# Optimization experiments

Measured on AMD Instinct MI355X. Metric: run time of the kernel, lower is better.

The kernel has to match this reference:

```python
import jax, jax.numpy as jnp
import numpy as np

N = 6144
D = 128
TAU = 0.1
ADJ_P = 0.005  # edge density


def _l2_normalize(x, eps=1e-12):
    # matches torch F.normalize: x / max(||x||, eps)
    n = jnp.sqrt(jnp.sum(x * x, axis=-1, keepdims=True))
    return x / jnp.maximum(n, eps)


def setup_inputs() -> dict:
    key = jax.random.key(0)
    ks = jax.random.split(key, 8)
    embF = jax.random.normal(ks[0], (N, D), jnp.float32)
    embM = jax.random.normal(ks[1], (N, D), jnp.float32)
    embP = jax.random.normal(ks[2], (N, D), jnp.float32)
    FM_adj = (jax.random.uniform(ks[3], (N, N)) < ADJ_P).astype(jnp.float32)
    FP_adj = (jax.random.uniform(ks[4], (N, N)) < ADJ_P).astype(jnp.float32)
    W1 = jax.random.normal(ks[5], (2 * D, D), jnp.float32) * (1.0 / np.sqrt(2 * D))
    b1 = jnp.zeros((D,), jnp.float32)
    W2 = jax.random.normal(ks[6], (D, 2), jnp.float32) * (1.0 / np.sqrt(D))
    b2 = jnp.zeros((2,), jnp.float32)
    return {"embF": embF, "embM": embM, "embP": embP,
            "FM_adj": FM_adj, "FP_adj": FP_adj,
            "W1": W1, "b1": b1, "W2": W2, "b2": b2}


def reference(embF, embM, embP, FM_adj, FP_adj, W1, b1, W2, b2):
    # attention-weighted neighbor aggregation
    FM_repr = (FM_adj @ embM) / jnp.maximum(FM_adj.sum(1, keepdims=True), 1.0)
    FP_repr = (FP_adj @ embP) / jnp.maximum(FP_adj.sum(1, keepdims=True), 1.0)
    # stack(dim=1).view(N,-1) == concat along feature dim
    feat = jnp.concatenate([FM_repr, FP_repr], axis=1)            # [N, 2D]
    h = jnp.maximum(feat @ W1 + b1, 0.0)                           # ReLU (dropout inactive in eval)
    weights = jax.nn.softmax(h @ W2 + b2, axis=-1)                 # [N, 2]

    Fn = _l2_normalize(embF)
    Mn = _l2_normalize(embM)
    Pn = _l2_normalize(embP)

    FM_sim = jnp.exp((Fn @ Mn.T) / TAU)                            # [N, Nm]
    FP_sim = jnp.exp((Fn @ Pn.T) / TAU)                            # [N, Np]

    FM_pos = jnp.sum(FM_sim * FM_adj, axis=1)
    FP_pos = jnp.sum(FP_sim * FP_adj, axis=1)
    FM_neg = jnp.sum(FM_sim, axis=1) - FM_pos
    FP_neg = jnp.sum(FP_sim, axis=1) - FP_pos

    w0, w1w = weights[:, 0], weights[:, 1]
    wp = w0 * FM_pos + w1w * FP_pos
    wn = w0 * FM_neg + w1w * FP_neg

    nei_count = jnp.maximum(FM_adj.sum(1) + FP_adj.sum(1), 1.0)
    ratio = wp / (wp + wn) / nei_count
    ratio = jnp.maximum(ratio, 1e-10)
    loss = jnp.mean(-jnp.log(ratio))
    return loss, weights
```

## Files before the change

### kernel.cpp

```cpp
#include <hip/hip_runtime.h>
#include <hip/hip_bf16.h>

#define NN 6144
#define DD 128
#define PBL 136
#define INV_TAU 10.0f

typedef __attribute__((ext_vector_type(4))) float f32x4;
typedef __attribute__((ext_vector_type(8))) short s16x8;

__device__ __forceinline__ void ld4_async(const float4* p, float4& d) {
    asm volatile("global_load_dwordx4 %0, %1, off" : "=v"(d) : "v"(p));
}
__device__ __forceinline__ void vm_wait0() {
    asm volatile("s_waitcnt vmcnt(0)" ::: "memory");
}

__global__ void k_normalize(const float* __restrict__ embF,
                            const float* __restrict__ embM,
                            const float* __restrict__ embP,
                            const float* __restrict__ W1,
                            float* __restrict__ Fn,
                            float* __restrict__ rnM, float* __restrict__ rnP,
                            __hip_bfloat16* __restrict__ Fnb,
                            __hip_bfloat16* __restrict__ Mnb,
                            __hip_bfloat16* __restrict__ Pnb,
                            __hip_bfloat16* __restrict__ W1tb,
                            float* __restrict__ FMtot,
                            float* __restrict__ out) {
    int which = blockIdx.y;
    if (which == 3) {
        if (blockIdx.x < 128) {
            int n = blockIdx.x, c = threadIdx.x;
            W1tb[n * 256 + c] = __float2bfloat16(W1[c * DD + n]);
        } else if (blockIdx.x < 176) {
            int i = (blockIdx.x - 128) * 256 + threadIdx.x;
            FMtot[i] = 0.f;
        } else if (blockIdx.x == 176 && threadIdx.x == 0) {
            out[0] = 0.f;
        }
        return;
    }
    const float* src = which == 0 ? embF : (which == 1 ? embM : embP);
    __hip_bfloat16* dstb = which == 0 ? Fnb : (which == 1 ? Mnb : Pnb);
    int wave = threadIdx.x >> 6, lane = threadIdx.x & 63;
    int row = blockIdx.x * 4 + wave;
    float2 v = reinterpret_cast<const float2*>(src + (size_t)row * DD)[lane];
    float s = v.x * v.x + v.y * v.y;
#pragma unroll
    for (int m = 1; m <= 32; m <<= 1) s += __shfl_xor(s, m);
    float inv = 1.0f / fmaxf(sqrtf(s), 1e-12f);
    float2 o; o.x = v.x * inv; o.y = v.y * inv;
    if (which == 0)
        reinterpret_cast<float2*>(Fn + (size_t)row * DD)[lane] = o;
    if (lane == 0) {
        if (which == 1) rnM[row] = inv;
        if (which == 2) rnP[row] = inv;
    }
    __hip_bfloat162 ob;
    ob.x = __float2bfloat16(o.x);
    ob.y = __float2bfloat16(o.y);
    reinterpret_cast<__hip_bfloat162*>(dstb + (size_t)row * DD)[lane] = ob;
}

__device__ __forceinline__ void sparse_body(
        int unit, char* smem,
        const float* __restrict__ FM_adj, const float* __restrict__ FP_adj,
        const float* __restrict__ embM, const float* __restrict__ embP,
        const float* __restrict__ Fn,
        const float* __restrict__ rnM, const float* __restrict__ rnP,
        __hip_bfloat16* __restrict__ featb,
        float* __restrict__ FMpos, float* __restrict__ FPpos,
        float* __restrict__ cntF, float* __restrict__ cntP) {
    float* FnS = (float*)smem;
    int (*lbufT)[5] = (int(*)[5])(smem + 512);
    int* listS = (int*)(smem + 512 + 5120);
    float (*reprS)[DD] = (float(*)[DD])(smem + 512 + 5120 + 512);
    float* posS = (float*)(smem + 512 + 5120 + 512 + 4096);
    int* wvS = (int*)(smem + 512 + 5120 + 512 + 4096 + 32);
    int* Ktot = (int*)(smem + 512 + 5120 + 512 + 4096 + 32 + 16);

    const int row = unit >> 1, h = unit & 1;
    const float* adj  = h ? FP_adj : FM_adj;
    const float* embX = h ? embP : embM;
    const float* RN   = h ? rnP : rnM;
    const int tid = threadIdx.x, wv = tid >> 6, lane = tid & 63;

    if (tid < 32)
        reinterpret_cast<float4*>(FnS)[tid] =
            reinterpret_cast<const float4*>(Fn + (size_t)row * DD)[tid];

    const float4* rp = reinterpret_cast<const float4*>(adj + (size_t)row * NN);
    float4 v0, v1, v2, v3, v4, v5;
    ld4_async(rp + tid,        v0);
    ld4_async(rp + 256 + tid,  v1);
    ld4_async(rp + 512 + tid,  v2);
    ld4_async(rp + 768 + tid,  v3);
    ld4_async(rp + 1024 + tid, v4);
    ld4_async(rp + 1280 + tid, v5);
    vm_wait0();
    float4 vv[6] = {v0, v1, v2, v3, v4, v5};
    int mycnt = 0;
#pragma unroll
    for (int u = 0; u < 6; ++u) {
        int cb = (u * 256 + tid) * 4;
        if (vv[u].x != 0.f) { if (mycnt < 4) lbufT[tid][mycnt] = cb;     mycnt++; }
        if (vv[u].y != 0.f) { if (mycnt < 4) lbufT[tid][mycnt] = cb + 1; mycnt++; }
        if (vv[u].z != 0.f) { if (mycnt < 4) lbufT[tid][mycnt] = cb + 2; mycnt++; }
        if (vv[u].w != 0.f) { if (mycnt < 4) lbufT[tid][mycnt] = cb + 3; mycnt++; }
    }
    int cnt = mycnt < 4 ? mycnt : 4;
    int x = cnt;
#pragma unroll
    for (int d = 1; d < 64; d <<= 1) {
        int y = __shfl_up(x, d);
        if (lane >= d) x += y;
    }
    int t = mycnt;
#pragma unroll
    for (int msk = 1; msk <= 32; msk <<= 1) t += __shfl_xor(t, msk);
    if (tid == 0) Ktot[1] = 0;
    if (lane == 63) wvS[wv] = x;
    __syncthreads();
    if (lane == 0) atomicAdd(&Ktot[1], t);
    if (tid == 0) {
        int s = 0;
#pragma unroll
        for (int i = 0; i < 4; ++i) { int v = wvS[i]; wvS[i] = s; s += v; }
        Ktot[0] = s < 128 ? s : 128;
    }
    __syncthreads();
    int off = wvS[wv] + (x - cnt);
    for (int i = 0; i < cnt; ++i) {
        int s = off + i;
        if (s < 128) listS[s] = lbufT[tid][i];
    }
    __syncthreads();
    const int K = Ktot[0];
    const float trueK = (float)Ktot[1];

    const int hw = tid >> 5, sl = tid & 31;
    float4 f4 = reinterpret_cast<const float4*>(FnS)[sl];
    float4 racc = {0.f, 0.f, 0.f, 0.f};
    float wsum = 0.f;
    for (int k = hw; k < K; k += 8) {
        int j = listS[k];
        float rn = RN[j];
        float4 e = reinterpret_cast<const float4*>(embX + (size_t)j * DD)[sl];
        racc.x += e.x; racc.y += e.y; racc.z += e.z; racc.w += e.w;
        float d = f4.x * e.x + f4.y * e.y + f4.z * e.z + f4.w * e.w;
#pragma unroll
        for (int msk = 1; msk <= 16; msk <<= 1) d += __shfl_xor(d, msk);
        wsum += __expf(d * rn * INV_TAU);
    }
    reinterpret_cast<float4*>(&reprS[hw][0])[sl] = racc;
    if (sl == 0) posS[hw] = wsum;
    __syncthreads();
    if (tid < DD) {
        float s = 0.f;
#pragma unroll
        for (int i = 0; i < 8; ++i) s += reprS[i][tid];
        featb[(size_t)row * (2 * DD) + h * DD + tid] =
            __float2bfloat16(s / fmaxf(trueK, 1.0f));
    }
    if (tid == 0) {
        float p = 0.f;
#pragma unroll
        for (int i = 0; i < 8; ++i) p += posS[i];
        (h ? FPpos : FMpos)[row] = p;
        (h ? cntP : cntF)[row] = trueK;
    }
}

__device__ __forceinline__ void dense_body(
        int unit, char* smem,
        const __hip_bfloat16* __restrict__ Fnb,
        const __hip_bfloat16* __restrict__ Mnb,
        const __hip_bfloat16* __restrict__ Pnb,
        float* __restrict__ FMtot, float* __restrict__ FPtot) {
    __hip_bfloat16 (*Bs)[PBL] = (__hip_bfloat16(*)[PBL])smem;
    const int bx = unit % 48, by = (unit / 48) % 16, half = unit / 768;
    const __hip_bfloat16* Bnb = half ? Pnb : Mnb;
    float* TOT = half ? FPtot : FMtot;
    const int tid = threadIdx.x;
    const int w = tid >> 6, lane = tid & 63;
    const int m = lane & 15, q = lane >> 4;
    const int rb = bx * 128 + w * 32;
    const int j0 = by * (NN / 16);

    s16x8 a[2][4];
#pragma unroll
    for (int g = 0; g < 2; ++g)
#pragma unroll
        for (int ks = 0; ks < 4; ++ks)
            a[g][ks] = *reinterpret_cast<const s16x8*>(
                Fnb + (size_t)(rb + g * 16 + m) * DD + ks * 32 + q * 8);

    float4 s0, s1, s2, s3;
    auto issue = [&](int jc) {
        const float4* gp = reinterpret_cast<const float4*>(Bnb + (size_t)jc * DD);
        ld4_async(gp + tid,       s0);
        ld4_async(gp + 256 + tid, s1);
        ld4_async(gp + 512 + tid, s2);
        ld4_async(gp + 768 + tid, s3);
    };
    auto stash = [&](int idx, const float4& v) {
        *reinterpret_cast<float4*>(&Bs[idx >> 4][(idx & 15) * 8]) = v;
    };

    issue(j0);
    float tot[2][4] = {{0.f, 0.f, 0.f, 0.f}, {0.f, 0.f, 0.f, 0.f}};
    for (int it = 0; it < 6; ++it) {
        vm_wait0();
        __syncthreads();
        stash(tid, s0);
        stash(256 + tid, s1);
        stash(512 + tid, s2);
        stash(768 + tid, s3);
        __syncthreads();
        if (it + 1 < 6) issue(j0 + (it + 1) * 64);
#pragma unroll
        for (int t = 0; t < 4; ++t) {
            s16x8 b[4];
#pragma unroll
            for (int ks = 0; ks < 4; ++ks)
                b[ks] = *reinterpret_cast<const s16x8*>(
                    &Bs[t * 16 + m][ks * 32 + q * 8]);
#pragma unroll
            for (int g = 0; g < 2; ++g) {
                f32x4 acc = {0.f, 0.f, 0.f, 0.f};
#pragma unroll
                for (int ks = 0; ks < 4; ++ks)
                    acc = __builtin_amdgcn_mfma_f32_16x16x32_bf16(
                        a[g][ks], b[ks], acc, 0, 0, 0);
#pragma unroll
                for (int r = 0; r < 4; ++r)
                    tot[g][r] += __expf(acc[r] * INV_TAU);
            }
        }
    }
#pragma unroll
    for (int msk = 1; msk <= 8; msk <<= 1)
#pragma unroll
        for (int g = 0; g < 2; ++g)
#pragma unroll
            for (int r = 0; r < 4; ++r)
                tot[g][r] += __shfl_xor(tot[g][r], msk);
    if (m == 0)
#pragma unroll
        for (int g = 0; g < 2; ++g)
#pragma unroll
            for (int r = 0; r < 4; ++r)
                atomicAdd(&TOT[rb + g * 16 + q * 4 + r], tot[g][r]);
}

__global__ __launch_bounds__(256) void k_main(
        const float* __restrict__ FM_adj, const float* __restrict__ FP_adj,
        const float* __restrict__ embM, const float* __restrict__ embP,
        const float* __restrict__ Fn,
        const float* __restrict__ rnM, const float* __restrict__ rnP,
        const __hip_bfloat16* __restrict__ Fnb,
        const __hip_bfloat16* __restrict__ Mnb,
        const __hip_bfloat16* __restrict__ Pnb,
        __hip_bfloat16* __restrict__ featb,
        float* __restrict__ FMpos, float* __restrict__ FPpos,
        float* __restrict__ FMtot, float* __restrict__ FPtot,
        float* __restrict__ cntF, float* __restrict__ cntP) {
    __shared__ char smem[64 * PBL * 2];
    const int b = blockIdx.x;
    const int u = b / 9, r = b - u * 9;
    if (r == 8)
        dense_body(u, smem, Fnb, Mnb, Pnb, FMtot, FPtot);
    else
        sparse_body(u * 8 + r, smem, FM_adj, FP_adj, embM, embP,
                    Fn, rnM, rnP, featb, FMpos, FPpos, cntF, cntP);
}

__global__ __launch_bounds__(256) void k_post(
        const __hip_bfloat16* __restrict__ featb,
        const __hip_bfloat16* __restrict__ W1tb,
        const float* __restrict__ b1, const float* __restrict__ W2,
        const float* __restrict__ b2,
        const float* __restrict__ FMpos, const float* __restrict__ FPpos,
        const float* __restrict__ FMtot, const float* __restrict__ FPtot,
        const float* __restrict__ cntF, const float* __restrict__ cntP,
        float* __restrict__ out) {
    __shared__ float zred[4][16][2];
    const int tid = threadIdx.x, w = tid >> 6, lane = tid & 63;
    const int m = lane & 15, q = lane >> 4;
    const int rb = blockIdx.x * 16;
    const int n0a = w * 32, n0b = w * 32 + 16;
    f32x4 accA = {0.f, 0.f, 0.f, 0.f}, accB = {0.f, 0.f, 0.f, 0.f};
#pragma unroll
    for (int ks = 0; ks < 8; ++ks) {
        s16x8 a = *reinterpret_cast<const s16x8*>(
            featb + (size_t)(rb + m) * 256 + ks * 32 + q * 8);
        s16x8 bA = *reinterpret_cast<const s16x8*>(
            W1tb + (size_t)(n0a + m) * 256 + ks * 32 + q * 8);
        s16x8 bB = *reinterpret_cast<const s16x8*>(
            W1tb + (size_t)(n0b + m) * 256 + ks * 32 + q * 8);
        accA = __builtin_amdgcn_mfma_f32_16x16x32_bf16(a, bA, accA, 0, 0, 0);
        accB = __builtin_amdgcn_mfma_f32_16x16x32_bf16(a, bB, accB, 0, 0, 0);
    }
    const float biasA = b1[n0a + m], biasB = b1[n0b + m];
    const float wA0 = W2[2 * (n0a + m)], wA1 = W2[2 * (n0a + m) + 1];
    const float wB0 = W2[2 * (n0b + m)], wB1 = W2[2 * (n0b + m) + 1];
#pragma unroll
    for (int r = 0; r < 4; ++r) {
        float hA = fmaxf(accA[r] + biasA, 0.f);
        float hB = fmaxf(accB[r] + biasB, 0.f);
        float p0 = hA * wA0 + hB * wB0;
        float p1 = hA * wA1 + hB * wB1;
#pragma unroll
        for (int msk = 1; msk <= 8; msk <<= 1) {
            p0 += __shfl_xor(p0, msk);
            p1 += __shfl_xor(p1, msk);
        }
        if (m == 0) {
            zred[w][q * 4 + r][0] = p0;
            zred[w][q * 4 + r][1] = p1;
        }
    }
    __syncthreads();
    if (tid < 16) {
        const int row = rb + tid;
        float z0 = zred[0][tid][0] + zred[1][tid][0]
                 + zred[2][tid][0] + zred[3][tid][0] + b2[0];
        float z1 = zred[0][tid][1] + zred[1][tid][1]
                 + zred[2][tid][1] + zred[3][tid][1] + b2[1];
        float mx = fmaxf(z0, z1);
        float e0 = expf(z0 - mx), e1 = expf(z1 - mx);
        float inv = 1.0f / (e0 + e1);
        float w0 = e0 * inv, w1 = e1 * inv;
        out[1 + row * 2 + 0] = w0;
        out[1 + row * 2 + 1] = w1;
        float wp = w0 * FMpos[row] + w1 * FPpos[row];
        float wn = w0 * (FMtot[row] - FMpos[row]) + w1 * (FPtot[row] - FPpos[row]);
        float nei = fmaxf(cntF[row] + cntP[row], 1.0f);
        float ratio = fmaxf(wp / (wp + wn) / nei, 1e-10f);
        float term = -logf(ratio);
#pragma unroll
        for (int msk = 1; msk <= 8; msk <<= 1) term += __shfl_xor(term, msk);
        if (tid == 0) atomicAdd(out, term * (1.0f / NN));
    }
}

extern "C" void kernel_launch(void* const* d_in, const int* in_sizes, int n_in,
                              void* d_out, int out_size, void* d_ws, size_t ws_size,
                              hipStream_t stream) {
    const float* embF   = (const float*)d_in[0];
    const float* embM   = (const float*)d_in[1];
    const float* embP   = (const float*)d_in[2];
    const float* FM_adj = (const float*)d_in[3];
    const float* FP_adj = (const float*)d_in[4];
    const float* W1     = (const float*)d_in[5];
    const float* b1     = (const float*)d_in[6];
    const float* W2     = (const float*)d_in[7];
    const float* b2     = (const float*)d_in[8];
    float* out = (float*)d_out;

    float* ws = (float*)d_ws;
    float* FMtot = ws;
    float* FPtot = FMtot + NN;
    float* zbuf  = FPtot + NN;
    float* FMpos = zbuf + 2 * NN;
    float* FPpos = FMpos + NN;
    float* cntF  = FPpos + NN;
    float* cntP  = cntF + NN;
    float* rnM   = cntP + NN;
    float* rnP   = rnM + NN;
    float* Fn    = rnP + NN;
    __hip_bfloat16* Fnb = (__hip_bfloat16*)(Fn + (size_t)NN * DD);
    __hip_bfloat16* Mnb = Fnb + (size_t)NN * DD;
    __hip_bfloat16* Pnb = Mnb + (size_t)NN * DD;
    __hip_bfloat16* featb = Pnb + (size_t)NN * DD;
    __hip_bfloat16* W1tb  = featb + (size_t)NN * 256;

    k_normalize<<<dim3(NN / 4, 4), 256, 0, stream>>>(embF, embM, embP, W1,
                                                     Fn, rnM, rnP,
                                                     Fnb, Mnb, Pnb, W1tb,
                                                     FMtot, out);
    k_main<<<dim3(13824), 256, 0, stream>>>(FM_adj, FP_adj, embM, embP,
                                            Fn, rnM, rnP, Fnb, Mnb, Pnb,
                                            featb, FMpos, FPpos, FMtot, FPtot,
                                            cntF, cntP);
    k_post<<<dim3(NN / 16), 256, 0, stream>>>(featb, W1tb, b1, W2, b2,
                                              FMpos, FPpos, FMtot, FPtot,
                                              cntF, cntP, out);
}
```

Baseline: 360.6 us.

## Process both adjacency halves per block, overlapping FP row load with FM processing

Each sparse block now handles one row for both FM and FP adjacency instead of one half, issuing all twelve row loads plus the Fn row up front. It waits only for the first seven loads, processes the FM half, then waits for the rest and processes FP. The Fn row goes straight into registers instead of through shared memory. This hides the FP load latency behind FM work and halves the sparse block count, at the cost of more registers per thread and fewer blocks available to hide latency.

```diff
diff --git a/kernel.cpp b/kernel.cpp
--- a/kernel.cpp
+++ b/kernel.cpp
@@ -14,6 +14,11 @@
 }
 __device__ __forceinline__ void vm_wait0() {
     asm volatile("s_waitcnt vmcnt(0)" ::: "memory");
+    __builtin_amdgcn_sched_barrier(0);
+}
+__device__ __forceinline__ void vm_wait6() {
+    asm volatile("s_waitcnt vmcnt(6)" ::: "memory");
+    __builtin_amdgcn_sched_barrier(0);
 }
 
 __global__ void k_normalize(const float* __restrict__ embF,
@@ -63,51 +68,32 @@
     reinterpret_cast<__hip_bfloat162*>(dstb + (size_t)row * DD)[lane] = ob;
 }
 
-__device__ __forceinline__ void sparse_body(
-        int unit, char* smem,
-        const float* __restrict__ FM_adj, const float* __restrict__ FP_adj,
+__device__ __forceinline__ void process_half(
+        int row, int h, const float4* va, float4 f4, char* smem,
         const float* __restrict__ embM, const float* __restrict__ embP,
-        const float* __restrict__ Fn,
         const float* __restrict__ rnM, const float* __restrict__ rnP,
         __hip_bfloat16* __restrict__ featb,
         float* __restrict__ FMpos, float* __restrict__ FPpos,
         float* __restrict__ cntF, float* __restrict__ cntP) {
-    float* FnS = (float*)smem;
-    int (*lbufT)[5] = (int(*)[5])(smem + 512);
-    int* listS = (int*)(smem + 512 + 5120);
-    float (*reprS)[DD] = (float(*)[DD])(smem + 512 + 5120 + 512);
-    float* posS = (float*)(smem + 512 + 5120 + 512 + 4096);
-    int* wvS = (int*)(smem + 512 + 5120 + 512 + 4096 + 32);
-    int* Ktot = (int*)(smem + 512 + 5120 + 512 + 4096 + 32 + 16);
-
-    const int row = unit >> 1, h = unit & 1;
-    const float* adj  = h ? FP_adj : FM_adj;
+    int (*lbufT)[5] = (int(*)[5])smem;
+    int* listS = (int*)(smem + 5120);
+    float (*reprS)[DD] = (float(*)[DD])(smem + 5632);
+    float* posS = (float*)(smem + 9728);
+    int* wvS = (int*)(smem + 9760);
+    int* Ktot = (int*)(smem + 9776);
+
     const float* embX = h ? embP : embM;
     const float* RN   = h ? rnP : rnM;
     const int tid = threadIdx.x, wv = tid >> 6, lane = tid & 63;
 
-    if (tid < 32)
-        reinterpret_cast<float4*>(FnS)[tid] =
-            reinterpret_cast<const float4*>(Fn + (size_t)row * DD)[tid];
-
-    const float4* rp = reinterpret_cast<const float4*>(adj + (size_t)row * NN);
-    float4 v0, v1, v2, v3, v4, v5;
-    ld4_async(rp + tid,        v0);
-    ld4_async(rp + 256 + tid,  v1);
-    ld4_async(rp + 512 + tid,  v2);
-    ld4_async(rp + 768 + tid,  v3);
-    ld4_async(rp + 1024 + tid, v4);
-    ld4_async(rp + 1280 + tid, v5);
-    vm_wait0();
-    float4 vv[6] = {v0, v1, v2, v3, v4, v5};
     int mycnt = 0;
 #pragma unroll
     for (int u = 0; u < 6; ++u) {
         int cb = (u * 256 + tid) * 4;
-        if (vv[u].x != 0.f) { if (mycnt < 4) lbufT[tid][mycnt] = cb;     mycnt++; }
-        if (vv[u].y != 0.f) { if (mycnt < 4) lbufT[tid][mycnt] = cb + 1; mycnt++; }
-        if (vv[u].z != 0.f) { if (mycnt < 4) lbufT[tid][mycnt] = cb + 2; mycnt++; }
-        if (vv[u].w != 0.f) { if (mycnt < 4) lbufT[tid][mycnt] = cb + 3; mycnt++; }
+        if (va[u].x != 0.f) { if (mycnt < 4) lbufT[tid][mycnt] = cb;     mycnt++; }
+        if (va[u].y != 0.f) { if (mycnt < 4) lbufT[tid][mycnt] = cb + 1; mycnt++; }
+        if (va[u].z != 0.f) { if (mycnt < 4) lbufT[tid][mycnt] = cb + 2; mycnt++; }
+        if (va[u].w != 0.f) { if (mycnt < 4) lbufT[tid][mycnt] = cb + 3; mycnt++; }
     }
     int cnt = mycnt < 4 ? mycnt : 4;
     int x = cnt;
@@ -140,7 +126,6 @@
     const float trueK = (float)Ktot[1];
 
     const int hw = tid >> 5, sl = tid & 31;
-    float4 f4 = reinterpret_cast<const float4*>(FnS)[sl];
     float4 racc = {0.f, 0.f, 0.f, 0.f};
     float wsum = 0.f;
     for (int k = hw; k < K; k += 8) {
@@ -268,12 +253,41 @@
         float* __restrict__ cntF, float* __restrict__ cntP) {
     __shared__ char smem[64 * PBL * 2];
     const int b = blockIdx.x;
-    const int u = b / 9, r = b - u * 9;
-    if (r == 8)
+    const int u = b / 5, r = b - u * 5;
+    if (r == 4) {
         dense_body(u, smem, Fnb, Mnb, Pnb, FMtot, FPtot);
-    else
-        sparse_body(u * 8 + r, smem, FM_adj, FP_adj, embM, embP,
-                    Fn, rnM, rnP, featb, FMpos, FPpos, cntF, cntP);
+        return;
+    }
+    const int row = u * 4 + r;
+    const int tid = threadIdx.x;
+    const float4* rpA = reinterpret_cast<const float4*>(FM_adj + (size_t)row * NN);
+    const float4* rpB = reinterpret_cast<const float4*>(FP_adj + (size_t)row * NN);
+    float4 a0, a1, a2, a3, a4, a5, b0, b1, b2, b3, b4, b5, f4;
+    ld4_async(rpA + tid,        a0);
+    ld4_async(rpA + 256 + tid,  a1);
+    ld4_async(rpA + 512 + tid,  a2);
+    ld4_async(rpA + 768 + tid,  a3);
+    ld4_async(rpA + 1024 + tid, a4);
+    ld4_async(rpA + 1280 + tid, a5);
+    ld4_async(reinterpret_cast<const float4*>(Fn + (size_t)row * DD) + (tid & 31), f4);
+    ld4_async(rpB + tid,        b0);
+    ld4_async(rpB + 256 + tid,  b1);
+    ld4_async(rpB + 512 + tid,  b2);
+    ld4_async(rpB + 768 + tid,  b3);
+    ld4_async(rpB + 1024 + tid, b4);
+    ld4_async(rpB + 1280 + tid, b5);
+    vm_wait6();
+    {
+        float4 va[6] = {a0, a1, a2, a3, a4, a5};
+        process_half(row, 0, va, f4, smem, embM, embP, rnM, rnP,
+                     featb, FMpos, FPpos, cntF, cntP);
+    }
+    vm_wait0();
+    {
+        float4 vb[6] = {b0, b1, b2, b3, b4, b5};
+        process_half(row, 1, vb, f4, smem, embM, embP, rnM, rnP,
+                     featb, FMpos, FPpos, cntF, cntP);
+    }
 }
 
 __global__ __launch_bounds__(256) void k_post(
@@ -380,10 +394,10 @@
                                                      Fn, rnM, rnP,
                                                      Fnb, Mnb, Pnb, W1tb,
                                                      FMtot, out);
-    k_main<<<dim3(13824), 256, 0, stream>>>(FM_adj, FP_adj, embM, embP,
-                                            Fn, rnM, rnP, Fnb, Mnb, Pnb,
-                                            featb, FMpos, FPpos, FMtot, FPtot,
-                                            cntF, cntP);
+    k_main<<<dim3(7680), 256, 0, stream>>>(FM_adj, FP_adj, embM, embP,
+                                           Fn, rnM, rnP, Fnb, Mnb, Pnb,
+                                           featb, FMpos, FPpos, FMtot, FPtot,
+                                           cntF, cntP);
     k_post<<<dim3(NN / 16), 256, 0, stream>>>(featb, W1tb, b1, W2, b2,
                                               FMpos, FPpos, FMtot, FPtot,
                                               cntF, cntP, out);
```

New measurement: 360.9 us. Within noise of the previous version (+0.1%).

## Pipeline adjacency row loads into LDS with producer wave in persistent sparse blocks

Applied to the files above, without the earlier changes.

Sparse blocks now each process four rows (eight row-halves) sequentially. A dedicated producer wave streams the next adjacency row into a double-buffered LDS region via global_load_lds while the other three waves do neighbor gathering. The goal is to overlap the dense adjacency reads with compute and cut per-block launch overhead. In exchange, shared memory grows to about 58 KB per block, including dense blocks, which lowers occupancy, and fewer waves are left to do the gather work.

```diff
diff --git a/kernel.cpp b/kernel.cpp
--- a/kernel.cpp
+++ b/kernel.cpp
@@ -14,6 +14,16 @@
 }
 __device__ __forceinline__ void vm_wait0() {
     asm volatile("s_waitcnt vmcnt(0)" ::: "memory");
+}
+__device__ __forceinline__ void bar_lgkm() {
+    asm volatile("s_waitcnt lgkmcnt(0)" ::: "memory");
+    __builtin_amdgcn_s_barrier();
+    __builtin_amdgcn_sched_barrier(0);
+}
+__device__ __forceinline__ void gl_lds16(const float* g, float* l) {
+    __builtin_amdgcn_global_load_lds(
+        (const __attribute__((address_space(1))) void*)g,
+        (__attribute__((address_space(3))) void*)l, 16, 0, 0);
 }
 
 __global__ void k_normalize(const float* __restrict__ embF,
@@ -63,115 +73,6 @@
     reinterpret_cast<__hip_bfloat162*>(dstb + (size_t)row * DD)[lane] = ob;
 }
 
-__device__ __forceinline__ void sparse_body(
-        int unit, char* smem,
-        const float* __restrict__ FM_adj, const float* __restrict__ FP_adj,
-        const float* __restrict__ embM, const float* __restrict__ embP,
-        const float* __restrict__ Fn,
-        const float* __restrict__ rnM, const float* __restrict__ rnP,
-        __hip_bfloat16* __restrict__ featb,
-        float* __restrict__ FMpos, float* __restrict__ FPpos,
-        float* __restrict__ cntF, float* __restrict__ cntP) {
-    float* FnS = (float*)smem;
-    int (*lbufT)[5] = (int(*)[5])(smem + 512);
-    int* listS = (int*)(smem + 512 + 5120);
-    float (*reprS)[DD] = (float(*)[DD])(smem + 512 + 5120 + 512);
-    float* posS = (float*)(smem + 512 + 5120 + 512 + 4096);
-    int* wvS = (int*)(smem + 512 + 5120 + 512 + 4096 + 32);
-    int* Ktot = (int*)(smem + 512 + 5120 + 512 + 4096 + 32 + 16);
-
-    const int row = unit >> 1, h = unit & 1;
-    const float* adj  = h ? FP_adj : FM_adj;
-    const float* embX = h ? embP : embM;
-    const float* RN   = h ? rnP : rnM;
-    const int tid = threadIdx.x, wv = tid >> 6, lane = tid & 63;
-
-    if (tid < 32)
-        reinterpret_cast<float4*>(FnS)[tid] =
-            reinterpret_cast<const float4*>(Fn + (size_t)row * DD)[tid];
-
-    const float4* rp = reinterpret_cast<const float4*>(adj + (size_t)row * NN);
-    float4 v0, v1, v2, v3, v4, v5;
-    ld4_async(rp + tid,        v0);
-    ld4_async(rp + 256 + tid,  v1);
-    ld4_async(rp + 512 + tid,  v2);
-    ld4_async(rp + 768 + tid,  v3);
-    ld4_async(rp + 1024 + tid, v4);
-    ld4_async(rp + 1280 + tid, v5);
-    vm_wait0();
-    float4 vv[6] = {v0, v1, v2, v3, v4, v5};
-    int mycnt = 0;
-#pragma unroll
-    for (int u = 0; u < 6; ++u) {
-        int cb = (u * 256 + tid) * 4;
-        if (vv[u].x != 0.f) { if (mycnt < 4) lbufT[tid][mycnt] = cb;     mycnt++; }
-        if (vv[u].y != 0.f) { if (mycnt < 4) lbufT[tid][mycnt] = cb + 1; mycnt++; }
-        if (vv[u].z != 0.f) { if (mycnt < 4) lbufT[tid][mycnt] = cb + 2; mycnt++; }
-        if (vv[u].w != 0.f) { if (mycnt < 4) lbufT[tid][mycnt] = cb + 3; mycnt++; }
-    }
-    int cnt = mycnt < 4 ? mycnt : 4;
-    int x = cnt;
-#pragma unroll
-    for (int d = 1; d < 64; d <<= 1) {
-        int y = __shfl_up(x, d);
-        if (lane >= d) x += y;
-    }
-    int t = mycnt;
-#pragma unroll
-    for (int msk = 1; msk <= 32; msk <<= 1) t += __shfl_xor(t, msk);
-    if (tid == 0) Ktot[1] = 0;
-    if (lane == 63) wvS[wv] = x;
-    __syncthreads();
-    if (lane == 0) atomicAdd(&Ktot[1], t);
-    if (tid == 0) {
-        int s = 0;
-#pragma unroll
-        for (int i = 0; i < 4; ++i) { int v = wvS[i]; wvS[i] = s; s += v; }
-        Ktot[0] = s < 128 ? s : 128;
-    }
-    __syncthreads();
-    int off = wvS[wv] + (x - cnt);
-    for (int i = 0; i < cnt; ++i) {
-        int s = off + i;
-        if (s < 128) listS[s] = lbufT[tid][i];
-    }
-    __syncthreads();
-    const int K = Ktot[0];
-    const float trueK = (float)Ktot[1];
-
-    const int hw = tid >> 5, sl = tid & 31;
-    float4 f4 = reinterpret_cast<const float4*>(FnS)[sl];
-    float4 racc = {0.f, 0.f, 0.f, 0.f};
-    float wsum = 0.f;
-    for (int k = hw; k < K; k += 8) {
-        int j = listS[k];
-        float rn = RN[j];
-        float4 e = reinterpret_cast<const float4*>(embX + (size_t)j * DD)[sl];
-        racc.x += e.x; racc.y += e.y; racc.z += e.z; racc.w += e.w;
-        float d = f4.x * e.x + f4.y * e.y + f4.z * e.z + f4.w * e.w;
-#pragma unroll
-        for (int msk = 1; msk <= 16; msk <<= 1) d += __shfl_xor(d, msk);
-        wsum += __expf(d * rn * INV_TAU);
-    }
-    reinterpret_cast<float4*>(&reprS[hw][0])[sl] = racc;
-    if (sl == 0) posS[hw] = wsum;
-    __syncthreads();
-    if (tid < DD) {
-        float s = 0.f;
-#pragma unroll
-        for (int i = 0; i < 8; ++i) s += reprS[i][tid];
-        featb[(size_t)row * (2 * DD) + h * DD + tid] =
-            __float2bfloat16(s / fmaxf(trueK, 1.0f));
-    }
-    if (tid == 0) {
-        float p = 0.f;
-#pragma unroll
-        for (int i = 0; i < 8; ++i) p += posS[i];
-        (h ? FPpos : FMpos)[row] = p;
-        (h ? cntP : cntF)[row] = trueK;
-    }
-}
-
 __device__ __forceinline__ void dense_body(
         int unit, char* smem,
         const __hip_bfloat16* __restrict__ Fnb,
@@ -266,14 +167,125 @@
         float* __restrict__ FMpos, float* __restrict__ FPpos,
         float* __restrict__ FMtot, float* __restrict__ FPtot,
         float* __restrict__ cntF, float* __restrict__ cntP) {
-    __shared__ char smem[64 * PBL * 2];
+    __shared__ char smem[58432];
     const int b = blockIdx.x;
-    const int u = b / 9, r = b - u * 9;
-    if (r == 8)
-        dense_body(u, smem, Fnb, Mnb, Pnb, FMtot, FPtot);
-    else
-        sparse_body(u * 8 + r, smem, FM_adj, FP_adj, embM, embP,
-                    Fn, rnM, rnP, featb, FMpos, FPpos, cntF, cntP);
+    if (b & 1) {
+        dense_body(b >> 1, smem, Fnb, Mnb, Pnb, FMtot, FPtot);
+        return;
+    }
+    int (*lbufT)[5] = (int(*)[5])(smem + 49152);
+    int* listS = (int*)(smem + 54272);
+    float* FnS = (float*)(smem + 54784);
+    float (*reprS)[DD] = (float(*)[DD])(smem + 55296);
+    float* posS = (float*)(smem + 58368);
+    int* wvS = (int*)(smem + 58392);
+    int* Ktot = (int*)(smem + 58408);
+
+    const int sb = b >> 1;
+    const int row0 = sb * 4;
+    const int tid = threadIdx.x, wv = tid >> 6, lane = tid & 63;
+
+    auto stage = [&](int u, float* dst) {
+        int rr = row0 + (u >> 1);
+        const float* src = ((u & 1) ? FP_adj : FM_adj) + (size_t)rr * NN;
+        const float* g = src + (lane << 2);
+#pragma unroll
+        for (int k = 0; k < 24; ++k)
+            gl_lds16(g + k * 256, dst + k * 256);
+    };
+
+    if (wv == 3) { stage(0, (float*)smem); vm_wait0(); }
+    bar_lgkm();
+
+    for (int u = 0; u < 8; ++u) {
+        const int cur = u & 1;
+        const int row = row0 + (u >> 1), h = u & 1;
+        if (wv == 3 && u + 1 < 8)
+            stage(u + 1, (float*)(smem + (size_t)(cur ^ 1) * 24576));
+
+        if (tid < 32)
+            reinterpret_cast<float4*>(FnS)[tid] =
+                reinterpret_cast<const float4*>(Fn + (size_t)row * DD)[tid];
+
+        const float4* bc = (const float4*)(smem + (size_t)cur * 24576);
+        int mycnt = 0;
+#pragma unroll
+        for (int uu = 0; uu < 6; ++uu) {
+            float4 v = bc[uu * 256 + tid];
+            int cb = (uu * 256 + tid) * 4;
+            if (v.x != 0.f) { if (mycnt < 4) lbufT[tid][mycnt] = cb;     mycnt++; }
+            if (v.y != 0.f) { if (mycnt < 4) lbufT[tid][mycnt] = cb + 1; mycnt++; }
+            if (v.z != 0.f) { if (mycnt < 4) lbufT[tid][mycnt] = cb + 2; mycnt++; }
+            if (v.w != 0.f) { if (mycnt < 4) lbufT[tid][mycnt] = cb + 3; mycnt++; }
+        }
+        int cnt = mycnt < 4 ? mycnt : 4;
+        int x = cnt;
+#pragma unroll
+        for (int d = 1; d < 64; d <<= 1) {
+            int y = __shfl_up(x, d);
+            if (lane >= d) x += y;
+        }
+        int t = mycnt;
+#pragma unroll
+        for (int msk = 1; msk <= 32; msk <<= 1) t += __shfl_xor(t, msk);
+        if (tid == 0) Ktot[1] = 0;
+        if (lane == 63) wvS[wv] = x;
+        bar_lgkm();
+        if (lane == 0) atomicAdd(&Ktot[1], t);
+        if (tid == 0) {
+            int s = 0;
+#pragma unroll
+            for (int i = 0; i < 4; ++i) { int v = wvS[i]; wvS[i] = s; s += v; }
+            Ktot[0] = s < 128 ? s : 128;
+        }
+        bar_lgkm();
+        int off = wvS[wv] + (x - cnt);
+        for (int i = 0; i < cnt; ++i) {
+            int s = off + i;
+            if (s < 128) listS[s] = lbufT[tid][i];
+        }
+        bar_lgkm();
+        const int K = Ktot[0];
+        const float trueK = (float)Ktot[1];
+
+        if (wv < 3) {
+            const float* embX = h ? embP : embM;
+            const float* RN   = h ? rnP : rnM;
+            const int hw = tid >> 5, sl = tid & 31;
+            float4 f4 = reinterpret_cast<const float4*>(FnS)[sl];
+            float4 racc = {0.f, 0.f, 0.f, 0.f};
+            float wsum = 0.f;
+            for (int k = hw; k < K; k += 6) {
+                int j = listS[k];
+                float rn = RN[j];
+                float4 e = reinterpret_cast<const float4*>(embX + (size_t)j * DD)[sl];
+                racc.x += e.x; racc.y += e.y; racc.z += e.z; racc.w += e.w;
+                float d = f4.x * e.x + f4.y * e.y + f4.z * e.z + f4.w * e.w;
+#pragma unroll
+                for (int msk = 1; msk <= 16; msk <<= 1) d += __shfl_xor(d, msk);
+                wsum += __expf(d * rn * INV_TAU);
+            }
+            reinterpret_cast<float4*>(&reprS[hw][0])[sl] = racc;
+            if (sl == 0) posS[hw] = wsum;
+        }
+        bar_lgkm();
+        if (tid < DD) {
+            float s = 0.f;
+#pragma unroll
+            for (int i = 0; i < 6; ++i) s += reprS[i][tid];
+            featb[(size_t)row * (2 * DD) + h * DD + tid] =
+                __float2bfloat16(s / fmaxf(trueK, 1.0f));
+        }
+        if (tid == 0) {
+            float p = 0.f;
+#pragma unroll
+            for (int i = 0; i < 6; ++i) p += posS[i];
+            (h ? FPpos : FMpos)[row] = p;
+            (h ? cntP : cntF)[row] = trueK;
+        }
+        if (wv == 3) vm_wait0();
+        bar_lgkm();
+    }
 }
 
 __global__ __launch_bounds__(256) void k_post(
@@ -380,10 +392,10 @@
                                                      Fn, rnM, rnP,
                                                      Fnb, Mnb, Pnb, W1tb,
                                                      FMtot, out);
-    k_main<<<dim3(13824), 256, 0, stream>>>(FM_adj, FP_adj, embM, embP,
-                                            Fn, rnM, rnP, Fnb, Mnb, Pnb,
-                                            featb, FMpos, FPpos, FMtot, FPtot,
-                                            cntF, cntP);
+    k_main<<<dim3(3072), 256, 0, stream>>>(FM_adj, FP_adj, embM, embP,
+                                           Fn, rnM, rnP, Fnb, Mnb, Pnb,
+                                           featb, FMpos, FPpos, FMtot, FPtot,
+                                           cntF, cntP);
     k_post<<<dim3(NN / 16), 256, 0, stream>>>(featb, W1tb, b1, W2, b2,
                                               FMpos, FPpos, FMtot, FPtot,
                                               cntF, cntP, out);
```

After: 531.0 us. 47.3% more time.
